# Performance work log

Hardware: AMD Instinct MI355X
Metric: run time of the kernel (lower is better)

Reference implementation:

```python
import jax, jax.numpy as jnp
import numpy as np

N = 5_000_000   # total nodes
B = 16384       # number of graphs
F_X = 4
F_U = 1


def setup_inputs() -> dict:
    key = jax.random.key(0)
    k = jax.random.split(key, 6)
    x = jax.random.normal(k[0], (N, F_X), dtype=jnp.float32)
    batch = jnp.sort(jax.random.randint(k[1], (N,), 0, B)).astype(jnp.int64)
    u = jax.random.normal(k[2], (B, F_U), dtype=jnp.float32)
    d = F_U + F_X  # 5
    W1 = jax.random.normal(k[3], (d, d), dtype=jnp.float32) / np.sqrt(d)
    b1 = jnp.zeros((d,), dtype=jnp.float32)
    W2 = jax.random.normal(k[4], (d, F_U), dtype=jnp.float32) / np.sqrt(d)
    b2 = jnp.zeros((F_U,), dtype=jnp.float32)
    return {"x": x, "batch": batch, "u": u, "W1": W1, "b1": b1, "W2": W2, "b2": b2}


def reference(x, batch, u, W1, b1, W2, b2):
    # scatter_mean(x, batch, dim=0): segment sum / segment count (empty -> 0)
    seg_sum = jax.ops.segment_sum(x, batch, num_segments=B)            # [B, F_x]
    cnt = jax.ops.segment_sum(jnp.ones((x.shape[0],), x.dtype), batch,
                              num_segments=B)                          # [B]
    mean = jnp.where(cnt[:, None] > 0, seg_sum / jnp.maximum(cnt, 1.0)[:, None], 0.0)
    h = jnp.concatenate([u, mean], axis=1)                             # [B, 5]
    h = jax.nn.leaky_relu(h @ W1 + b1, negative_slope=0.1)
    return h @ W2 + b2                                                 # [B, 1]
```

## Files before the change

kernel.cpp:

```cpp
#include <hip/hip_runtime.h>

#define WAVE 64

__global__ void seg_reduce_kernel(const float4* __restrict__ x,
                                  const int* __restrict__ batch,
                                  float* __restrict__ seg_sum,
                                  float* __restrict__ seg_cnt,
                                  int N, int per_wave) {
    const int wid  = (blockIdx.x * blockDim.x + threadIdx.x) / WAVE;
    const int lane = threadIdx.x & (WAVE - 1);

    long long start = (long long)wid * per_wave;
    long long end   = start + per_wave;
    if (end > N) end = N;
    if (start >= N) return;

    for (long long base = start; base < end; base += WAVE) {
        long long idx = base + lane;
        const bool valid = (idx < end);

        int   seg = valid ? batch[idx] : -1;
        float4 v  = valid ? x[idx] : make_float4(0.f, 0.f, 0.f, 0.f);
        float  c  = valid ? 1.0f : 0.0f;

        #pragma unroll
        for (int off = 1; off < WAVE; off <<= 1) {
            int   s2 = __shfl_down(seg, off);
            float vx = __shfl_down(v.x, off);
            float vy = __shfl_down(v.y, off);
            float vz = __shfl_down(v.z, off);
            float vw = __shfl_down(v.w, off);
            float c2 = __shfl_down(c,   off);
            if ((lane + off) < WAVE && s2 == seg) {
                v.x += vx; v.y += vy; v.z += vz; v.w += vw; c += c2;
            }
        }

        int seg_prev = __shfl_up(seg, 1);
        bool head = valid && (lane == 0 || seg_prev != seg);
        if (head) {
            atomicAdd(&seg_sum[(long long)seg * 4 + 0], v.x);
            atomicAdd(&seg_sum[(long long)seg * 4 + 1], v.y);
            atomicAdd(&seg_sum[(long long)seg * 4 + 2], v.z);
            atomicAdd(&seg_sum[(long long)seg * 4 + 3], v.w);
            atomicAdd(&seg_cnt[seg], c);
        }
    }
}

__global__ void mlp_kernel(const float* __restrict__ u,
                           const float* __restrict__ W1,
                           const float* __restrict__ b1,
                           const float* __restrict__ W2,
                           const float* __restrict__ b2,
                           const float* __restrict__ seg_sum,
                           const float* __restrict__ seg_cnt,
                           float* __restrict__ out, int B) {
    int b = blockIdx.x * blockDim.x + threadIdx.x;
    if (b >= B) return;

    float c   = seg_cnt[b];
    float inv = (c > 0.5f) ? (1.0f / c) : 0.0f;
    float4 s  = ((const float4*)seg_sum)[b];

    float h[5];
    h[0] = u[b];
    h[1] = s.x * inv;
    h[2] = s.y * inv;
    h[3] = s.z * inv;
    h[4] = s.w * inv;

    float o = b2[0];
    #pragma unroll
    for (int j = 0; j < 5; ++j) {
        float t = b1[j];
        #pragma unroll
        for (int i = 0; i < 5; ++i) t += h[i] * W1[i * 5 + j];
        t = (t > 0.0f) ? t : 0.1f * t;
        o += t * W2[j];
    }
    out[b] = o;
}

extern "C" void kernel_launch(void* const* d_in, const int* in_sizes, int n_in,
                              void* d_out, int out_size, void* d_ws, size_t ws_size,
                              hipStream_t stream) {
    const float* x     = (const float*)d_in[0];
    const int*   batch = (const int*)  d_in[1];
    const float* u     = (const float*)d_in[2];
    const float* W1    = (const float*)d_in[3];
    const float* b1    = (const float*)d_in[4];
    const float* W2    = (const float*)d_in[5];
    const float* b2    = (const float*)d_in[6];
    float* out = (float*)d_out;

    const int N = in_sizes[0] / 4;
    const int B = out_size;

    float* seg_sum = (float*)d_ws;
    float* seg_cnt = seg_sum + (size_t)B * 4;

    hipMemsetAsync(d_ws, 0, (size_t)B * 5 * sizeof(float), stream);

    const int threads = 256;
    const int blocks  = 1024;
    const int waves   = blocks * threads / WAVE;
    int per_wave = ((N + waves - 1) / waves + (WAVE - 1)) & ~(WAVE - 1);

    seg_reduce_kernel<<<blocks, threads, 0, stream>>>(
        (const float4*)x, batch, seg_sum, seg_cnt, N, per_wave);

    mlp_kernel<<<(B + 255) / 256, 256, 0, stream>>>(
        u, W1, b1, W2, b2, seg_sum, seg_cnt, out, B);
}
```

Before: 154.2 us.

## Replace atomic segmented scan with boundary search and per-segment wave reduction fused with MLP

Rewrites the segment mean so a first kernel finds segment start offsets from the sorted batch array, and a second kernel assigns one wave per graph to sum its contiguous rows and then apply the MLP directly. This removes the per-chunk segmented shuffle scan, the global atomics, the workspace memset and the separate MLP launch. It relies on batch being sorted, and reads batch in a separate pass. Each wave handles about 300 rows with float4 loads, which may leave load balance and tail lanes uneven.

```diff
diff --git a/kernel.cpp b/kernel.cpp
--- a/kernel.cpp
+++ b/kernel.cpp
@@ -2,84 +2,68 @@
 
 #define WAVE 64
 
-__global__ void seg_reduce_kernel(const float4* __restrict__ x,
-                                  const int* __restrict__ batch,
-                                  float* __restrict__ seg_sum,
-                                  float* __restrict__ seg_cnt,
-                                  int N, int per_wave) {
+__global__ void find_starts_kernel(const int* __restrict__ batch,
+                                   int* __restrict__ seg_start,
+                                   int N, int B) {
+    int i = blockIdx.x * blockDim.x + threadIdx.x;
+    if (i > N) return;
+    int b_prev = (i == 0) ? -1 : batch[i - 1];
+    int b_cur  = (i == N) ? B  : batch[i];
+    for (int s = b_prev + 1; s <= b_cur; ++s) seg_start[s] = i;
+}
+
+__global__ void __launch_bounds__(256)
+seg_mean_mlp_kernel(const float4* __restrict__ x,
+                    const int* __restrict__ seg_start,
+                    const float* __restrict__ u,
+                    const float* __restrict__ W1,
+                    const float* __restrict__ b1,
+                    const float* __restrict__ W2,
+                    const float* __restrict__ b2,
+                    float* __restrict__ out, int B) {
     const int wid  = (blockIdx.x * blockDim.x + threadIdx.x) / WAVE;
     const int lane = threadIdx.x & (WAVE - 1);
+    if (wid >= B) return;
 
-    long long start = (long long)wid * per_wave;
-    long long end   = start + per_wave;
-    if (end > N) end = N;
-    if (start >= N) return;
+    const int start = seg_start[wid];
+    const int end   = seg_start[wid + 1];
 
-    for (long long base = start; base < end; base += WAVE) {
-        long long idx = base + lane;
-        const bool valid = (idx < end);
+    float4 acc = make_float4(0.f, 0.f, 0.f, 0.f);
+    for (int i = start + lane; i < end; i += WAVE) {
+        float4 v = x[i];
+        acc.x += v.x; acc.y += v.y; acc.z += v.z; acc.w += v.w;
+    }
 
-        int   seg = valid ? batch[idx] : -1;
-        float4 v  = valid ? x[idx] : make_float4(0.f, 0.f, 0.f, 0.f);
-        float  c  = valid ? 1.0f : 0.0f;
+    #pragma unroll
+    for (int off = 32; off > 0; off >>= 1) {
+        acc.x += __shfl_down(acc.x, off);
+        acc.y += __shfl_down(acc.y, off);
+        acc.z += __shfl_down(acc.z, off);
+        acc.w += __shfl_down(acc.w, off);
+    }
 
+    if (lane == 0) {
+        const int cnt = end - start;
+        const float inv = (cnt > 0) ? (1.0f / (float)cnt) : 0.0f;
+
+        float h[5];
+        h[0] = u[wid];
+        h[1] = acc.x * inv;
+        h[2] = acc.y * inv;
+        h[3] = acc.z * inv;
+        h[4] = acc.w * inv;
+
+        float o = b2[0];
         #pragma unroll
-        for (int off = 1; off < WAVE; off <<= 1) {
-            int   s2 = __shfl_down(seg, off);
-            float vx = __shfl_down(v.x, off);
-            float vy = __shfl_down(v.y, off);
-            float vz = __shfl_down(v.z, off);
-            float vw = __shfl_down(v.w, off);
-            float c2 = __shfl_down(c,   off);
-            if ((lane + off) < WAVE && s2 == seg) {
-                v.x += vx; v.y += vy; v.z += vz; v.w += vw; c += c2;
-            }
+        for (int j = 0; j < 5; ++j) {
+            float t = b1[j];
+            #pragma unroll
+            for (int i = 0; i < 5; ++i) t += h[i] * W1[i * 5 + j];
+            t = (t > 0.0f) ? t : 0.1f * t;
+            o += t * W2[j];
         }
-
-        int seg_prev = __shfl_up(seg, 1);
-        bool head = valid && (lane == 0 || seg_prev != seg);
-        if (head) {
-            atomicAdd(&seg_sum[(long long)seg * 4 + 0], v.x);
-            atomicAdd(&seg_sum[(long long)seg * 4 + 1], v.y);
-            atomicAdd(&seg_sum[(long long)seg * 4 + 2], v.z);
-            atomicAdd(&seg_sum[(long long)seg * 4 + 3], v.w);
-            atomicAdd(&seg_cnt[seg], c);
-        }
+        out[wid] = o;
     }
-}
-
-__global__ void mlp_kernel(const float* __restrict__ u,
-                           const float* __restrict__ W1,
-                           const float* __restrict__ b1,
-                           const float* __restrict__ W2,
-                           const float* __restrict__ b2,
-                           const float* __restrict__ seg_sum,
-                           const float* __restrict__ seg_cnt,
-                           float* __restrict__ out, int B) {
-    int b = blockIdx.x * blockDim.x + threadIdx.x;
-    if (b >= B) return;
-
-    float c   = seg_cnt[b];
-    float inv = (c > 0.5f) ? (1.0f / c) : 0.0f;
-    float4 s  = ((const float4*)seg_sum)[b];
-
-    float h[5];
-    h[0] = u[b];
-    h[1] = s.x * inv;
-    h[2] = s.y * inv;
-    h[3] = s.z * inv;
-    h[4] = s.w * inv;
-
-    float o = b2[0];
-    #pragma unroll
-    for (int j = 0; j < 5; ++j) {
-        float t = b1[j];
-        #pragma unroll
-        for (int i = 0; i < 5; ++i) t += h[i] * W1[i * 5 + j];
-        t = (t > 0.0f) ? t : 0.1f * t;
-        o += t * W2[j];
-    }
-    out[b] = o;
 }
 
 extern "C" void kernel_launch(void* const* d_in, const int* in_sizes, int n_in,
@@ -97,19 +81,12 @@
     const int N = in_sizes[0] / 4;
     const int B = out_size;
 
-    float* seg_sum = (float*)d_ws;
-    float* seg_cnt = seg_sum + (size_t)B * 4;
+    int* seg_start = (int*)d_ws;
 
-    hipMemsetAsync(d_ws, 0, (size_t)B * 5 * sizeof(float), stream);
+    find_starts_kernel<<<(N + 1 + 255) / 256, 256, 0, stream>>>(batch, seg_start, N, B);
 
     const int threads = 256;
-    const int blocks  = 1024;
-    const int waves   = blocks * threads / WAVE;
-    int per_wave = ((N + waves - 1) / waves + (WAVE - 1)) & ~(WAVE - 1);
-
-    seg_reduce_kernel<<<blocks, threads, 0, stream>>>(
-        (const float4*)x, batch, seg_sum, seg_cnt, N, per_wave);
-
-    mlp_kernel<<<(B + 255) / 256, 256, 0, stream>>>(
-        u, W1, b1, W2, b2, seg_sum, seg_cnt, out, B);
+    const int blocks  = (B * WAVE + threads - 1) / threads;
+    seg_mean_mlp_kernel<<<blocks, threads, 0, stream>>>(
+        (const float4*)x, seg_start, u, W1, b1, W2, b2, out, B);
 }
```

Result: faster. 148.0 us (-4.0%).
